# Kernel tuning notes

Measured on AMD Instinct MI355X. Metric: run time of the kernel, lower is better.

## Reference

```python
import jax, jax.numpy as jnp
import numpy as np

TOP_K = 13
NUM_CLASSES = 80
ALPHA = 1.0
BETA = 6.0
EPS = 1e-9


def setup_inputs() -> dict:
    key = jax.random.key(0)
    ks = jax.random.split(key, 8)
    BS, A, C, N = 32, 8400, 80, 48
    pd_scores = jax.random.uniform(ks[0], (BS, A, C), jnp.float32)
    # well-formed predicted boxes (x1<x2, y1<y2) in [0,1]
    plt = jax.random.uniform(ks[1], (BS, A, 2), jnp.float32) * 0.7
    pwh = jax.random.uniform(ks[2], (BS, A, 2), jnp.float32) * 0.3 + 1e-3
    pd_bbox_es = jnp.concatenate([plt, plt + pwh], axis=-1)
    anc_points = jax.random.uniform(ks[3], (A, 2), jnp.float32)
    gt_labels = jax.random.randint(ks[4], (BS, N, 1), 0, C)
    glt = jax.random.uniform(ks[5], (BS, N, 2), jnp.float32) * 0.7
    gwh = jax.random.uniform(ks[6], (BS, N, 2), jnp.float32) * 0.3 + 1e-3
    gt_bbox_es = jnp.concatenate([glt, glt + gwh], axis=-1)
    mask_gt = jnp.ones((BS, N, 1), jnp.float32)
    return {"pd_scores": pd_scores, "pd_bbox_es": pd_bbox_es,
            "anc_points": anc_points, "gt_labels": gt_labels,
            "gt_bbox_es": gt_bbox_es, "mask_gt": mask_gt}


def _cal_iou(box_a, box_b):
    # box_a: (b, n, 1, 4), box_b: (b, 1, A, 4) -> (b, n, A, 1)
    a_x1, a_y1, a_x2, a_y2 = jnp.split(box_a, 4, axis=-1)
    b_x1, b_y1, b_x2, b_y2 = jnp.split(box_b, 4, axis=-1)
    w1, h1 = a_x2 - a_x1, a_y2 - a_y1 + 1e-9  # matches torch: eps on h only
    w2, h2 = b_x2 - b_x1, b_y2 - b_y1 + 1e-9
    inter = (jnp.minimum(a_x2, b_x2) - jnp.maximum(a_x1, b_x1)).clip(0) * \
            (jnp.minimum(a_y2, b_y2) - jnp.maximum(a_y1, b_y1)).clip(0)
    union = w1 * h1 + w2 * h2 - inter + 1e-9
    return inter / union


def _forward(pd_scores, pd_bbox_es, anc_points, gt_labels, gt_bbox_es, mask_gt):
    bs, A, C = pd_scores.shape
    n = gt_bbox_es.shape[1]
    dt = pd_scores.dtype

    # ---- box metrics (vectorized, non-roll-out path) ----
    overlaps = _cal_iou(gt_bbox_es[:, :, None, :], pd_bbox_es[:, None, :, :])[..., 0].clip(0.)  # (b,n,A)
    labels = gt_labels[..., 0]  # (b, n) int
    # bbox_scores[b, j, a] = pd_scores[b, a, labels[b, j]]
    bbox_scores = pd_scores[jnp.arange(bs)[:, None], :, labels]  # (b, n, A)
    align_metric = (bbox_scores ** ALPHA) * (overlaps ** BETA)

    # ---- anchors inside gt boxes ----
    lt = gt_bbox_es[:, :, None, :2]   # (b, n, 1, 2)
    rb = gt_bbox_es[:, :, None, 2:]
    deltas = jnp.concatenate([anc_points[None, None] - lt, rb - anc_points[None, None]], axis=-1)  # (b,n,A,4)
    mask_in_gts = (deltas.min(-1) > EPS).astype(dt)  # (b, n, A)

    # ---- top-k candidates ----
    metrics = align_metric * mask_in_gts
    _, topk_idx = jax.lax.top_k(metrics, TOP_K)  # (b, n, k)
    topk_mask = jnp.broadcast_to(mask_gt > 0, topk_idx.shape)
    topk_idx = jnp.where(topk_mask, topk_idx, 0)
    bi = jnp.arange(bs)[:, None, None]
    ni = jnp.arange(n)[None, :, None]
    counts = jnp.zeros((bs, n, A), jnp.int32).at[bi, ni, topk_idx].add(1)
    is_in_topk = jnp.where(counts > 1, 0, counts).astype(dt)  # (b, n, A)

    mask_pos = is_in_topk * mask_in_gts * mask_gt  # (b, n, A)

    # ---- resolve anchors assigned to multiple gts by max overlap ----
    fg_mask = mask_pos.sum(axis=1)  # (b, A)
    mask_multi = fg_mask[:, None, :] > 1  # (b, 1->n, A)
    max_overlaps_idx = jnp.argmax(overlaps, axis=1)  # (b, A)
    is_max = jax.nn.one_hot(max_overlaps_idx, n, dtype=dt).transpose(0, 2, 1)  # (b, n, A)
    mask_pos = jnp.where(mask_multi, is_max, mask_pos)
    fg_mask = mask_pos.sum(axis=1)
    target_gt_idx = jnp.argmax(mask_pos, axis=1)  # (b, A)

    # ---- gather targets ----
    flat_idx = target_gt_idx + jnp.arange(bs)[:, None] * n  # (b, A)
    target_labels = gt_labels.reshape(-1)[flat_idx]          # (b, A)
    target_bbox_es = gt_bbox_es.reshape(-1, 4)[flat_idx]     # (b, A, 4)
    target_scores = jax.nn.one_hot(target_labels, NUM_CLASSES, dtype=dt)
    target_scores = jnp.where(fg_mask[..., None] > 0, target_scores, 0.)

    # ---- normalized alignment metric ----
    align_metric = align_metric * mask_pos
    pos_align_metrics = align_metric.max(axis=-1, keepdims=True)   # (b, n, 1)
    pos_overlaps = (overlaps * mask_pos).max(axis=-1, keepdims=True)
    norm_align_metric = (align_metric * pos_overlaps / (pos_align_metrics + EPS)).max(axis=1)[..., None]  # (b, A, 1)
    target_scores = target_scores * norm_align_metric

    return target_labels, target_bbox_es, target_scores, fg_mask > 0, target_gt_idx


def reference(pd_scores, pd_bbox_es, anc_points, gt_labels, gt_bbox_es, mask_gt):
    return _forward(pd_scores, pd_bbox_es, anc_points, gt_labels, gt_bbox_es, mask_gt)
```

## Files before the change

### kernel.cpp

```cpp
#include <hip/hip_runtime.h>

#define BS_ 32
#define A_  8400
#define C_  80
#define N_  48
#define K_  13
#define EPSF 1e-9f
#define CH_ 128
#define NCH_ 66
#define SEGS_ 33

__global__ __launch_bounds__(256) void tal_metrics(
    const float* __restrict__ ps, const float* __restrict__ pb,
    const float* __restrict__ anc, const int* __restrict__ gl,
    const float* __restrict__ gb, float* __restrict__ metrics)
{
    __shared__ float  s_sc[CH_ * 81];
    __shared__ float4 s_pb[CH_];
    __shared__ float2 s_anc[CH_];
    __shared__ float4 s_gt[N_];
    __shared__ int    s_lab[N_];

    const int b  = blockIdx.y;
    const int a0 = blockIdx.x * CH_;
    const int ca = min(CH_, A_ - a0);
    const int tid = threadIdx.x;

    if (tid < N_) {
        s_gt[tid]  = reinterpret_cast<const float4*>(gb)[b * N_ + tid];
        s_lab[tid] = gl[b * N_ + tid];
    }
    if (tid < ca) {
        s_pb[tid]  = reinterpret_cast<const float4*>(pb)[(size_t)b * A_ + a0 + tid];
        s_anc[tid] = reinterpret_cast<const float2*>(anc)[a0 + tid];
    }
    const float4* src = reinterpret_cast<const float4*>(ps + ((size_t)b * A_ + a0) * C_);
    const int nf4 = ca * 20;
    for (int i = tid; i < nf4; i += 256) {
        float4 v = src[i];
        int a_l = i / 20, c = (i % 20) * 4;
        float* d = &s_sc[a_l * 81 + c];
        d[0] = v.x; d[1] = v.y; d[2] = v.z; d[3] = v.w;
    }
    __syncthreads();

    const int a_l = tid & (CH_ - 1);
    const int nh  = tid >> 7;
    if (a_l < ca) {
        float4 p = s_pb[a_l];
        float2 ap = s_anc[a_l];
        float wp = p.z - p.x, hp = p.w - p.y + EPSF;
        float areap = wp * hp;
        size_t outbase = (size_t)b * N_ * A_ + a0 + a_l;
        for (int n = nh; n < N_; n += 2) {
            float4 g = s_gt[n];
            float wg = g.z - g.x, hg = g.w - g.y + EPSF;
            float iw = fmaxf(fminf(g.z, p.z) - fmaxf(g.x, p.x), 0.f);
            float ih = fmaxf(fminf(g.w, p.w) - fmaxf(g.y, p.y), 0.f);
            float inter = iw * ih;
            float uni = wg * hg + areap - inter + EPSF;
            float ov = fmaxf(inter / uni, 0.f);
            float sc = s_sc[a_l * 81 + s_lab[n]];
            float o2 = ov * ov;
            float al = sc * (o2 * o2 * o2);
            float mind = fminf(fminf(ap.x - g.x, ap.y - g.y), fminf(g.z - ap.x, g.w - ap.y));
            metrics[outbase + (size_t)n * A_] = (mind > EPSF) ? al : 0.f;
        }
    }
}

__global__ __launch_bounds__(256) void tal_topk(
    const float* __restrict__ metrics, const float* __restrict__ anc,
    const float* __restrict__ gb, const float* __restrict__ mask_gt,
    int* __restrict__ fg_count, int* __restrict__ assigned_min)
{
    __shared__ __align__(16) float sm[SEGS_ * 256];
    __shared__ float seg_max[SEGS_];
    __shared__ int   s_topk[K_];

    const int bn = blockIdx.x;
    const int b  = bn / N_;
    const int n_idx = bn - b * N_;
    const int tid = threadIdx.x;
    const int lane = tid & 63;
    const int wid  = tid >> 6;

    const float4 g = reinterpret_cast<const float4*>(gb)[bn];
    const float mgt = mask_gt[bn];

    const float4* row4 = reinterpret_cast<const float4*>(metrics + (size_t)bn * A_);
    float4* sm4 = reinterpret_cast<float4*>(sm);
    for (int i = tid; i < A_ / 4; i += 256) sm4[i] = row4[i];
    if (tid < SEGS_ * 256 - A_) sm[A_ + tid] = -1.f;
    __syncthreads();

    for (int s = wid; s < SEGS_; s += 4) {
        float4 v = sm4[s * 64 + lane];
        float m = fmaxf(fmaxf(v.x, v.y), fmaxf(v.z, v.w));
        for (int o = 32; o; o >>= 1) m = fmaxf(m, __shfl_xor(m, o));
        if (lane == 0) seg_max[s] = m;
    }
    __syncthreads();

    if (wid == 0) {
        for (int k = 0; k < K_; ++k) {
            float v = (lane < SEGS_) ? seg_max[lane] : -3.f;
            int   i = lane;
            for (int o = 32; o; o >>= 1) {
                float v2 = __shfl_xor(v, o); int i2 = __shfl_xor(i, o);
                if (v2 > v || (v2 == v && i2 < i)) { v = v2; i = i2; }
            }
            const int s = i;
            float4 q = sm4[s * 64 + lane];
            float bv = q.x; int bj = 0;
            if (q.y > bv) { bv = q.y; bj = 1; }
            if (q.z > bv) { bv = q.z; bj = 2; }
            if (q.w > bv) { bv = q.w; bj = 3; }
            float wv = bv; int wi = (s << 8) + (lane << 2) + bj;
            for (int o = 32; o; o >>= 1) {
                float v2 = __shfl_xor(wv, o); int i2 = __shfl_xor(wi, o);
                if (v2 > wv || (v2 == wv && i2 < wi)) { wv = v2; wi = i2; }
            }
            if (((wi >> 2) & 63) == lane) {
                sm[wi] = -2.f;
                int comp = wi & 3;
                if (comp == 0) q.x = -2.f; else if (comp == 1) q.y = -2.f;
                else if (comp == 2) q.z = -2.f; else q.w = -2.f;
            }
            float nm = fmaxf(fmaxf(q.x, q.y), fmaxf(q.z, q.w));
            for (int o = 32; o; o >>= 1) nm = fmaxf(nm, __shfl_xor(nm, o));
            if (lane == 0) { seg_max[s] = nm; s_topk[k] = wi; }
        }
    }
    __syncthreads();

    if (tid < K_ && mgt > 0.f) {
        int a = s_topk[tid];
        float2 ap = reinterpret_cast<const float2*>(anc)[a];
        float mind = fminf(fminf(ap.x - g.x, ap.y - g.y), fminf(g.z - ap.x, g.w - ap.y));
        if (mind > EPSF) {
            atomicAdd(&fg_count[b * A_ + a], 1);
            atomicMin(&assigned_min[b * A_ + a], n_idx);
        }
    }
}

__device__ __forceinline__ float iou_f(float4 g, float4 p) {
    float wg = g.z - g.x, hg = g.w - g.y + EPSF;
    float wp = p.z - p.x, hp = p.w - p.y + EPSF;
    float iw = fmaxf(fminf(g.z, p.z) - fmaxf(g.x, p.x), 0.f);
    float ih = fmaxf(fminf(g.w, p.w) - fmaxf(g.y, p.y), 0.f);
    float inter = iw * ih;
    float uni = wg * hg + wp * hp - inter + EPSF;
    return fmaxf(inter / uni, 0.f);
}

__global__ __launch_bounds__(256) void tal_resolve(
    const float* __restrict__ metrics, const float* __restrict__ pb,
    const float* __restrict__ gb, const int* __restrict__ gl,
    const float* __restrict__ ps,
    const int* __restrict__ fg_count, const int* __restrict__ assigned_min,
    float* __restrict__ o_labels, float* __restrict__ o_bbox,
    float* __restrict__ o_fg, float* __restrict__ o_tgi,
    float* __restrict__ norm_num,
    unsigned int* __restrict__ pos_al, unsigned int* __restrict__ pos_ov)
{
    __shared__ float4 s_gt[N_];
    __shared__ int    s_lab[N_];
    const int b = blockIdx.y;
    const int a = blockIdx.x * 256 + threadIdx.x;
    if (threadIdx.x < N_) {
        s_gt[threadIdx.x]  = reinterpret_cast<const float4*>(gb)[b * N_ + threadIdx.x];
        s_lab[threadIdx.x] = gl[b * N_ + threadIdx.x];
    }
    __syncthreads();
    if (a >= A_) return;

    const int idx = b * A_ + a;
    const int fg = fg_count[idx];
    float al = 0.f, ov = 0.f, fgo = 0.f;
    int tgi = 0;
    if (fg == 1) {
        tgi = assigned_min[idx];
        al = metrics[((size_t)b * N_ + tgi) * A_ + a];
        float4 p = reinterpret_cast<const float4*>(pb)[(size_t)b * A_ + a];
        ov = iou_f(s_gt[tgi], p);
        fgo = 1.f;
    } else if (fg > 1) {
        float4 p = reinterpret_cast<const float4*>(pb)[(size_t)b * A_ + a];
        float bv = -1.f; int bi = 0;
        for (int n = 0; n < N_; ++n) {
            float v = iou_f(s_gt[n], p);
            if (v > bv) { bv = v; bi = n; }
        }
        tgi = bi; ov = bv;
        float sc = ps[((size_t)b * A_ + a) * C_ + s_lab[bi]];
        float o2 = ov * ov;
        al = sc * (o2 * o2 * o2);
        fgo = 1.f;
    }
    if (fgo > 0.f) {
        atomicMax(&pos_al[b * N_ + tgi], __float_as_uint(al));
        atomicMax(&pos_ov[b * N_ + tgi], __float_as_uint(ov));
    }
    o_fg[idx] = fgo;
    o_tgi[idx] = (float)tgi;
    o_labels[idx] = (float)s_lab[tgi];
    reinterpret_cast<float4*>(o_bbox)[idx] = s_gt[tgi];
    norm_num[idx] = al;
}

__global__ __launch_bounds__(256) void tal_scores(
    const float* __restrict__ o_labels, const float* __restrict__ o_fg,
    const float* __restrict__ o_tgi, const float* __restrict__ norm_num,
    const unsigned int* __restrict__ pos_al, const unsigned int* __restrict__ pos_ov,
    float* __restrict__ o_scores)
{
    const int idx = blockIdx.x * 256 + threadIdx.x;
    if (idx >= BS_ * A_ * (C_ / 4)) return;
    const int ba = idx / 20;
    const int c0 = (idx % 20) * 4;
    float4 v = {0.f, 0.f, 0.f, 0.f};
    if (o_fg[ba] > 0.f) {
        int lab = (int)o_labels[ba];
        if (lab >= c0 && lab < c0 + 4) {
            int b = ba / A_;
            int tgi = (int)o_tgi[ba];
            float pa = __uint_as_float(pos_al[b * N_ + tgi]);
            float po = __uint_as_float(pos_ov[b * N_ + tgi]);
            float nrm = norm_num[ba] * po / (pa + EPSF);
            if (lab == c0) v.x = nrm; else if (lab == c0 + 1) v.y = nrm;
            else if (lab == c0 + 2) v.z = nrm; else v.w = nrm;
        }
    }
    reinterpret_cast<float4*>(o_scores)[idx] = v;
}

extern "C" void kernel_launch(void* const* d_in, const int* in_sizes, int n_in,
                              void* d_out, int out_size, void* d_ws, size_t ws_size,
                              hipStream_t stream) {
    const float* pd_scores = (const float*)d_in[0];
    const float* pd_bbox   = (const float*)d_in[1];
    const float* anc       = (const float*)d_in[2];
    const int*   gt_labels = (const int*)d_in[3];
    const float* gt_bbox   = (const float*)d_in[4];
    const float* mask_gt   = (const float*)d_in[5];

    const size_t BA  = (size_t)BS_ * A_;
    const size_t BNA = (size_t)BS_ * N_ * A_;
    const int    BN  = BS_ * N_;

    float* out      = (float*)d_out;
    float* o_labels = out;
    float* o_bbox   = out + BA;
    float* o_scores = out + BA * 5;
    float* o_fg     = o_scores + BA * C_;
    float* o_tgi    = o_fg + BA;

    float* metrics        = (float*)d_ws;
    int*   fg_count       = (int*)(metrics + BNA);
    unsigned int* pos_al  = (unsigned int*)(fg_count + BA);
    unsigned int* pos_ov  = pos_al + BN;
    int*   assigned_min   = (int*)(pos_ov + BN);
    float* norm_num       = (float*)(assigned_min + BA);

    hipMemsetAsync(fg_count, 0, (BA + 2 * BN) * sizeof(int), stream);
    hipMemsetAsync(assigned_min, 0x7f, BA * sizeof(int), stream);

    tal_metrics<<<dim3(NCH_, BS_), 256, 0, stream>>>(
        pd_scores, pd_bbox, anc, gt_labels, gt_bbox, metrics);

    tal_topk<<<BN, 256, 0, stream>>>(
        metrics, anc, gt_bbox, mask_gt, fg_count, assigned_min);

    tal_resolve<<<dim3((A_ + 255) / 256, BS_), 256, 0, stream>>>(
        metrics, pd_bbox, gt_bbox, gt_labels, pd_scores,
        fg_count, assigned_min,
        o_labels, o_bbox, o_fg, o_tgi, norm_num, pos_al, pos_ov);

    tal_scores<<<(int)((BA * 20 + 255) / 256), 256, 0, stream>>>(
        o_labels, o_fg, o_tgi, norm_num, pos_al, pos_ov, o_scores);
}
```

Before: 268.1 us.

## Parallelize top-k across four waves with candidate merge; halve metrics chunk

The top-k kernel now has each of the four waves run its own 13-step selection over its interleaved subset of segments. Wave 0 then merges the 52 candidates with 13 wave-wide argmax passes, replacing the earlier single-wave serial loop over all 33 segments. Separately, the metrics kernel chunk size drops from 128 to 64 anchors per block, with each thread covering 12 GTs instead of 24, which doubles the block count. The top-k change removes the serial bottleneck where three waves sat idle. The tie-breaking order should stay the same, since the global index is used for ties.

```diff
diff --git a/kernel.cpp b/kernel.cpp
--- a/kernel.cpp
+++ b/kernel.cpp
@@ -6,9 +6,17 @@
 #define N_  48
 #define K_  13
 #define EPSF 1e-9f
-#define CH_ 128
-#define NCH_ 66
+#define CH_ 64
+#define NCH_ 132
 #define SEGS_ 33
+
+__device__ __forceinline__ void wave_argmax_tie(float& v, int& i) {
+    for (int o = 32; o; o >>= 1) {
+        float v2 = __shfl_xor(v, o);
+        int   i2 = __shfl_xor(i, o);
+        if (v2 > v || (v2 == v && i2 < i)) { v = v2; i = i2; }
+    }
+}
 
 __global__ __launch_bounds__(256) void tal_metrics(
     const float* __restrict__ ps, const float* __restrict__ pb,
@@ -45,14 +53,14 @@
     __syncthreads();
 
     const int a_l = tid & (CH_ - 1);
-    const int nh  = tid >> 7;
+    const int nh  = tid >> 6;
     if (a_l < ca) {
         float4 p = s_pb[a_l];
         float2 ap = s_anc[a_l];
         float wp = p.z - p.x, hp = p.w - p.y + EPSF;
         float areap = wp * hp;
         size_t outbase = (size_t)b * N_ * A_ + a0 + a_l;
-        for (int n = nh; n < N_; n += 2) {
+        for (int n = nh; n < N_; n += 4) {
             float4 g = s_gt[n];
             float wg = g.z - g.x, hg = g.w - g.y + EPSF;
             float iw = fmaxf(fminf(g.z, p.z) - fmaxf(g.x, p.x), 0.f);
@@ -76,6 +84,8 @@
 {
     __shared__ __align__(16) float sm[SEGS_ * 256];
     __shared__ float seg_max[SEGS_];
+    __shared__ float cand_v[4 * K_];
+    __shared__ int   cand_i[4 * K_];
     __shared__ int   s_topk[K_];
 
     const int bn = blockIdx.x;
@@ -83,7 +93,7 @@
     const int n_idx = bn - b * N_;
     const int tid = threadIdx.x;
     const int lane = tid & 63;
-    const int wid  = tid >> 6;
+    const int w    = tid >> 6;
 
     const float4 g = reinterpret_cast<const float4*>(gb)[bn];
     const float mgt = mask_gt[bn];
@@ -94,42 +104,46 @@
     if (tid < SEGS_ * 256 - A_) sm[A_ + tid] = -1.f;
     __syncthreads();
 
-    for (int s = wid; s < SEGS_; s += 4) {
+    const int nseg = (w == 0) ? 9 : 8;
+    for (int s = w; s < SEGS_; s += 4) {
         float4 v = sm4[s * 64 + lane];
         float m = fmaxf(fmaxf(v.x, v.y), fmaxf(v.z, v.w));
         for (int o = 32; o; o >>= 1) m = fmaxf(m, __shfl_xor(m, o));
         if (lane == 0) seg_max[s] = m;
     }
-    __syncthreads();
-
-    if (wid == 0) {
+
+    for (int k = 0; k < K_; ++k) {
+        float v  = (lane < nseg) ? seg_max[w + 4 * lane] : -3.f;
+        int   li = lane;
+        wave_argmax_tie(v, li);
+        const int s = w + 4 * li;
+        float4 q = sm4[s * 64 + lane];
+        float bv = q.x; int bj = 0;
+        if (q.y > bv) { bv = q.y; bj = 1; }
+        if (q.z > bv) { bv = q.z; bj = 2; }
+        if (q.w > bv) { bv = q.w; bj = 3; }
+        float wv = bv; int wi = (s << 8) + (lane << 2) + bj;
+        wave_argmax_tie(wv, wi);
+        if (((wi >> 2) & 63) == lane) {
+            sm[wi] = -2.f;
+            int c = wi & 3;
+            if (c == 0) q.x = -2.f; else if (c == 1) q.y = -2.f;
+            else if (c == 2) q.z = -2.f; else q.w = -2.f;
+        }
+        float nm = fmaxf(fmaxf(q.x, q.y), fmaxf(q.z, q.w));
+        for (int o = 32; o; o >>= 1) nm = fmaxf(nm, __shfl_xor(nm, o));
+        if (lane == 0) { seg_max[s] = nm; cand_v[w * K_ + k] = wv; cand_i[w * K_ + k] = wi; }
+    }
+    __syncthreads();
+
+    if (w == 0) {
+        float v   = (lane < 4 * K_) ? cand_v[lane] : -3.f;
+        int   idx = (lane < 4 * K_) ? cand_i[lane] : 0x7fffffff;
         for (int k = 0; k < K_; ++k) {
-            float v = (lane < SEGS_) ? seg_max[lane] : -3.f;
-            int   i = lane;
-            for (int o = 32; o; o >>= 1) {
-                float v2 = __shfl_xor(v, o); int i2 = __shfl_xor(i, o);
-                if (v2 > v || (v2 == v && i2 < i)) { v = v2; i = i2; }
-            }
-            const int s = i;
-            float4 q = sm4[s * 64 + lane];
-            float bv = q.x; int bj = 0;
-            if (q.y > bv) { bv = q.y; bj = 1; }
-            if (q.z > bv) { bv = q.z; bj = 2; }
-            if (q.w > bv) { bv = q.w; bj = 3; }
-            float wv = bv; int wi = (s << 8) + (lane << 2) + bj;
-            for (int o = 32; o; o >>= 1) {
-                float v2 = __shfl_xor(wv, o); int i2 = __shfl_xor(wi, o);
-                if (v2 > wv || (v2 == wv && i2 < wi)) { wv = v2; wi = i2; }
-            }
-            if (((wi >> 2) & 63) == lane) {
-                sm[wi] = -2.f;
-                int comp = wi & 3;
-                if (comp == 0) q.x = -2.f; else if (comp == 1) q.y = -2.f;
-                else if (comp == 2) q.z = -2.f; else q.w = -2.f;
-            }
-            float nm = fmaxf(fmaxf(q.x, q.y), fmaxf(q.z, q.w));
-            for (int o = 32; o; o >>= 1) nm = fmaxf(nm, __shfl_xor(nm, o));
-            if (lane == 0) { seg_max[s] = nm; s_topk[k] = wi; }
+            float mv = v; int mi = idx;
+            wave_argmax_tie(mv, mi);
+            if (idx == mi) v = -3.f;
+            if (lane == 0) s_topk[k] = mi;
         }
     }
     __syncthreads();
```

Measured after the change: 276.1 us. 1.03x slower.

## Replace shared-memory segmented top-k with per-lane register insertion lists

Applied to the files above, without the earlier changes.

The top-k kernel now assigns one 64-lane wavefront per (batch, gt) row instead of one block. Each lane streams the row from global memory and keeps a sorted 13-entry list of packed (value, ~index) 64-bit keys in registers. The lists are then merged with 13 rounds of wave shuffles. This removes the shared-memory staging, the segment-max passes and the block barriers. Separately, the metrics kernel chunk size drops from 128 to 64 anchors with four gt groups per block, which doubles the block count. The cost is heavy register use and 64-bit compare-and-swap chains per element.

```diff
diff --git a/kernel.cpp b/kernel.cpp
--- a/kernel.cpp
+++ b/kernel.cpp
@@ -6,9 +6,14 @@
 #define N_  48
 #define K_  13
 #define EPSF 1e-9f
-#define CH_ 128
-#define NCH_ 66
-#define SEGS_ 33
+#define CH_ 64
+#define NCH_ 132
+
+typedef unsigned long long u64k;
+
+__device__ __forceinline__ u64k pack_key(float v, int idx) {
+    return ((u64k)__float_as_uint(v) << 32) | (unsigned int)(~idx);
+}
 
 __global__ __launch_bounds__(256) void tal_metrics(
     const float* __restrict__ ps, const float* __restrict__ pb,
@@ -45,14 +50,14 @@
     __syncthreads();
 
     const int a_l = tid & (CH_ - 1);
-    const int nh  = tid >> 7;
+    const int nh  = tid >> 6;
     if (a_l < ca) {
         float4 p = s_pb[a_l];
         float2 ap = s_anc[a_l];
         float wp = p.z - p.x, hp = p.w - p.y + EPSF;
         float areap = wp * hp;
         size_t outbase = (size_t)b * N_ * A_ + a0 + a_l;
-        for (int n = nh; n < N_; n += 2) {
+        for (int n = nh; n < N_; n += 4) {
             float4 g = s_gt[n];
             float wg = g.z - g.x, hg = g.w - g.y + EPSF;
             float iw = fmaxf(fminf(g.z, p.z) - fmaxf(g.x, p.x), 0.f);
@@ -69,78 +74,61 @@
     }
 }
 
+#define INS1(L) { u64k mn = t < L ? t : L; u64k mx = t < L ? L : t; L = mx; t = mn; }
+#define INSERT(k) if ((k) > l12) { u64k t = (k); \
+    INS1(l0) INS1(l1) INS1(l2) INS1(l3) INS1(l4) INS1(l5) INS1(l6) \
+    INS1(l7) INS1(l8) INS1(l9) INS1(l10) INS1(l11) INS1(l12) }
+
 __global__ __launch_bounds__(256) void tal_topk(
     const float* __restrict__ metrics, const float* __restrict__ anc,
     const float* __restrict__ gb, const float* __restrict__ mask_gt,
     int* __restrict__ fg_count, int* __restrict__ assigned_min)
 {
-    __shared__ __align__(16) float sm[SEGS_ * 256];
-    __shared__ float seg_max[SEGS_];
-    __shared__ int   s_topk[K_];
-
-    const int bn = blockIdx.x;
-    const int b  = bn / N_;
-    const int n_idx = bn - b * N_;
-    const int tid = threadIdx.x;
-    const int lane = tid & 63;
-    const int wid  = tid >> 6;
-
-    const float4 g = reinterpret_cast<const float4*>(gb)[bn];
-    const float mgt = mask_gt[bn];
-
-    const float4* row4 = reinterpret_cast<const float4*>(metrics + (size_t)bn * A_);
-    float4* sm4 = reinterpret_cast<float4*>(sm);
-    for (int i = tid; i < A_ / 4; i += 256) sm4[i] = row4[i];
-    if (tid < SEGS_ * 256 - A_) sm[A_ + tid] = -1.f;
-    __syncthreads();
-
-    for (int s = wid; s < SEGS_; s += 4) {
-        float4 v = sm4[s * 64 + lane];
-        float m = fmaxf(fmaxf(v.x, v.y), fmaxf(v.z, v.w));
-        for (int o = 32; o; o >>= 1) m = fmaxf(m, __shfl_xor(m, o));
-        if (lane == 0) seg_max[s] = m;
-    }
-    __syncthreads();
-
-    if (wid == 0) {
-        for (int k = 0; k < K_; ++k) {
-            float v = (lane < SEGS_) ? seg_max[lane] : -3.f;
-            int   i = lane;
-            for (int o = 32; o; o >>= 1) {
-                float v2 = __shfl_xor(v, o); int i2 = __shfl_xor(i, o);
-                if (v2 > v || (v2 == v && i2 < i)) { v = v2; i = i2; }
-            }
-            const int s = i;
-            float4 q = sm4[s * 64 + lane];
-            float bv = q.x; int bj = 0;
-            if (q.y > bv) { bv = q.y; bj = 1; }
-            if (q.z > bv) { bv = q.z; bj = 2; }
-            if (q.w > bv) { bv = q.w; bj = 3; }
-            float wv = bv; int wi = (s << 8) + (lane << 2) + bj;
-            for (int o = 32; o; o >>= 1) {
-                float v2 = __shfl_xor(wv, o); int i2 = __shfl_xor(wi, o);
-                if (v2 > wv || (v2 == wv && i2 < wi)) { wv = v2; wi = i2; }
-            }
-            if (((wi >> 2) & 63) == lane) {
-                sm[wi] = -2.f;
-                int comp = wi & 3;
-                if (comp == 0) q.x = -2.f; else if (comp == 1) q.y = -2.f;
-                else if (comp == 2) q.z = -2.f; else q.w = -2.f;
-            }
-            float nm = fmaxf(fmaxf(q.x, q.y), fmaxf(q.z, q.w));
-            for (int o = 32; o; o >>= 1) nm = fmaxf(nm, __shfl_xor(nm, o));
-            if (lane == 0) { seg_max[s] = nm; s_topk[k] = wi; }
-        }
-    }
-    __syncthreads();
-
-    if (tid < K_ && mgt > 0.f) {
-        int a = s_topk[tid];
-        float2 ap = reinterpret_cast<const float2*>(anc)[a];
+    const int lane   = threadIdx.x & 63;
+    const int row_id = blockIdx.x * 4 + (threadIdx.x >> 6);
+    const int b      = row_id / N_;
+    const int n_idx  = row_id - b * N_;
+
+    const float4 g  = reinterpret_cast<const float4*>(gb)[row_id];
+    const float mgt = mask_gt[row_id];
+
+    const float4* row4 = reinterpret_cast<const float4*>(metrics + (size_t)row_id * A_);
+
+    u64k l0=0,l1=0,l2=0,l3=0,l4=0,l5=0,l6=0,l7=0,l8=0,l9=0,l10=0,l11=0,l12=0;
+
+    for (int i = 0; i < 33; ++i) {
+        int j = i * 64 + lane;
+        if (j < A_ / 4) {
+            float4 q = row4[j];
+            int e = j * 4;
+            u64k k0 = pack_key(q.x, e);
+            u64k k1 = pack_key(q.y, e + 1);
+            u64k k2 = pack_key(q.z, e + 2);
+            u64k k3 = pack_key(q.w, e + 3);
+            INSERT(k0) INSERT(k1) INSERT(k2) INSERT(k3)
+        }
+    }
+
+    int sel = -1;
+    for (int k = 0; k < K_; ++k) {
+        u64k w = l0;
+        for (int o = 32; o; o >>= 1) {
+            u64k w2 = __shfl_xor(w, o);
+            if (w2 > w) w = w2;
+        }
+        if (l0 == w) {
+            l0=l1; l1=l2; l2=l3; l3=l4; l4=l5; l5=l6; l6=l7;
+            l7=l8; l8=l9; l9=l10; l10=l11; l11=l12; l12=0;
+        }
+        if (lane == k) sel = ~((unsigned int)w);
+    }
+
+    if (lane < K_ && mgt > 0.f) {
+        float2 ap = reinterpret_cast<const float2*>(anc)[sel];
         float mind = fminf(fminf(ap.x - g.x, ap.y - g.y), fminf(g.z - ap.x, g.w - ap.y));
         if (mind > EPSF) {
-            atomicAdd(&fg_count[b * A_ + a], 1);
-            atomicMin(&assigned_min[b * A_ + a], n_idx);
+            atomicAdd(&fg_count[b * A_ + sel], 1);
+            atomicMin(&assigned_min[b * A_ + sel], n_idx);
         }
     }
 }
@@ -270,7 +258,7 @@
     tal_metrics<<<dim3(NCH_, BS_), 256, 0, stream>>>(
         pd_scores, pd_bbox, anc, gt_labels, gt_bbox, metrics);
 
-    tal_topk<<<BN, 256, 0, stream>>>(
+    tal_topk<<<BN / 4, 256, 0, stream>>>(
         metrics, anc, gt_bbox, mask_gt, fg_count, assigned_min);
 
     tal_resolve<<<dim3((A_ + 255) / 256, BS_), 256, 0, stream>>>(
```

Measured after the change: 286.2 us. +6.7%, slower.
